# Kernel optimization log

Hardware: AMD Instinct MI355X
Metric: run time of the kernel (lower is better)

The kernel has to match this reference:

```python
import jax, jax.numpy as jnp
import numpy as np

N_MESS = 50000
MAX_NEI = 8
INPUT_SIZE = 128
H_SIZE = 128
DEPTH = 5


def setup_inputs() -> dict:
    key = jax.random.key(0)
    ks = jax.random.split(key, 7)
    s = 0.05
    fmess = jax.random.normal(ks[0], (N_MESS, INPUT_SIZE), dtype=jnp.float32)
    bgraph = jax.random.randint(ks[1], (N_MESS, MAX_NEI), 0, N_MESS, dtype=jnp.int32)
    # torch nn.Linear weights are [out_features, in_features]
    W_z = jax.random.normal(ks[2], (H_SIZE, INPUT_SIZE + H_SIZE), dtype=jnp.float32) * s
    b_z = jnp.zeros((H_SIZE,), jnp.float32)
    W_r = jax.random.normal(ks[3], (H_SIZE, INPUT_SIZE), dtype=jnp.float32) * s  # no bias
    U_r = jax.random.normal(ks[4], (H_SIZE, H_SIZE), dtype=jnp.float32) * s
    b_Ur = jnp.zeros((H_SIZE,), jnp.float32)
    W_h = jax.random.normal(ks[5], (H_SIZE, INPUT_SIZE + H_SIZE), dtype=jnp.float32) * s
    b_h = jnp.zeros((H_SIZE,), jnp.float32)
    return {"fmess": fmess, "bgraph": bgraph, "W_z": W_z, "b_z": b_z,
            "W_r": W_r, "U_r": U_r, "b_Ur": b_Ur, "W_h": W_h, "b_h": b_h}


def _gru_step(fmess, h_nei, W_z, b_z, W_r, U_r, b_Ur, W_h, b_h):
    # h_nei: [N, K, H]
    sum_h = h_nei.sum(axis=1)                                     # [N, H]
    z = jax.nn.sigmoid(jnp.concatenate([fmess, sum_h], axis=1) @ W_z.T + b_z)
    r_1 = (fmess @ W_r.T)[:, None, :]                             # [N, 1, H]
    r_2 = jnp.einsum('nkh,gh->nkg', h_nei, U_r) + b_Ur            # [N, K, H]
    r = jax.nn.sigmoid(r_1 + r_2)
    sum_gated_h = (r * h_nei).sum(axis=1)                         # [N, H]
    pre_h = jnp.tanh(jnp.concatenate([fmess, sum_gated_h], axis=1) @ W_h.T + b_h)
    return (1.0 - z) * sum_h + z * pre_h


def reference(fmess, bgraph, W_z, b_z, W_r, U_r, b_Ur, W_h, b_h):
    n = fmess.shape[0]
    h = jnp.zeros((n, H_SIZE), dtype=fmess.dtype)
    mask = jnp.ones((n, 1), dtype=fmess.dtype).at[0, 0].set(0.0)  # message 0 is padding
    for _ in range(DEPTH):
        h_nei = h[bgraph]                                         # gather: [N, K, H]
        h = _gru_step(fmess, h_nei, W_z, b_z, W_r, U_r, b_Ur, W_h, b_h)
        h = h * mask
    return h
```

## Files before the change

### kernel.cpp

```cpp
#include <hip/hip_runtime.h>
#include <hip/hip_bf16.h>

#define NM 50000
#define HD 128
#define KNEI 8
#define BM 64
#define SPAD 136
#define NBLK ((NM + BM - 1) / BM)
#define NH ((size_t)NM * (size_t)HD)

typedef float  fx4   __attribute__((ext_vector_type(4)));
typedef short  s16x8 __attribute__((ext_vector_type(8)));
typedef short  s16x4 __attribute__((ext_vector_type(4)));

__device__ __forceinline__ float sigm_f(float x) {
    return __builtin_amdgcn_rcpf(1.0f + __expf(-x));
}
__device__ __forceinline__ float tanh_f(float x) {
    return 2.0f * sigm_f(2.0f * x) - 1.0f;
}
__device__ __forceinline__ unsigned short f2b(float f) {
    __hip_bfloat16 h = __float2bfloat16(f);
    return __builtin_bit_cast(unsigned short, h);
}
__device__ __forceinline__ float b2f(unsigned short u) {
    __hip_bfloat16 h = __builtin_bit_cast(__hip_bfloat16, u);
    return __bfloat162float(h);
}

#define MFMA16(a, b, c) __builtin_amdgcn_mfma_f32_16x16x32_bf16(a, b, c, 0, 0, 0)


__device__ __forceinline__ void stage_W16(const unsigned short* __restrict__ W16,
                                          int ldw, int woff,
                                          unsigned short (*Ws)[SPAD], int tid)
{
    const int g  = tid >> 1;
    const int c0 = (tid & 1) << 6;
    const unsigned short* src = W16 + (size_t)g * ldw + woff + c0;
    #pragma unroll
    for (int j = 0; j < 64; j += 8)
        *(s16x8*)&Ws[g][c0 + j] = *(const s16x8*)(src + j);
}

__device__ __forceinline__ void stage_A32(const float* __restrict__ A, int row0,
                                          unsigned short (*As)[SPAD], int tid)
{
    const int r  = tid & 63;
    const int c0 = (tid >> 6) << 5;
    int gr = row0 + r; if (gr >= NM) gr = NM - 1;
    const float* ap = A + (size_t)gr * HD + c0;
    #pragma unroll
    for (int j = 0; j < 32; j += 8) {
        s16x8 s;
        #pragma unroll
        for (int q = 0; q < 8; ++q) s[q] = (short)f2b(ap[j + q]);
        *(s16x8*)&As[r][c0 + j] = s;
    }
}

__device__ __forceinline__ void stage_A16(const unsigned short* __restrict__ A16, int row0,
                                          unsigned short (*As)[SPAD], int tid)
{
    const int r  = tid & 63;
    const int c0 = (tid >> 6) << 5;
    int gr = row0 + r; if (gr >= NM) gr = NM - 1;
    const unsigned short* ap = A16 + (size_t)gr * HD + c0;
    #pragma unroll
    for (int j = 0; j < 32; j += 8)
        *(s16x8*)&As[r][c0 + j] = *(const s16x8*)(ap + j);
}

__device__ __forceinline__ void lds_to_g16(const unsigned short (*L)[SPAD], int row0,
                                           unsigned short* __restrict__ G, int tid)
{
    const int r  = tid & 63;
    const int c0 = (tid >> 6) << 5;
    const int gr = row0 + r;
    if (gr >= NM) return;
    #pragma unroll
    for (int j = 0; j < 32; j += 8)
        *(s16x8*)&G[(size_t)gr * HD + c0 + j] = *(const s16x8*)&L[r][c0 + j];
}

__device__ __forceinline__ void mfma_128(const unsigned short (*As)[SPAD],
                                         const unsigned short (*Ws)[SPAD],
                                         int w, int l, fx4 (&acc)[8])
{
    const int rb = w * 16 + (l & 15);
    const int kq = (l >> 4) << 3;
    #pragma unroll
    for (int ks = 0; ks < 4; ++ks) {
        const s16x8 a = *(const s16x8*)&As[rb][ks * 32 + kq];
        #pragma unroll
        for (int nf = 0; nf < 8; ++nf) {
            const s16x8 b = *(const s16x8*)&Ws[nf * 16 + (l & 15)][ks * 32 + kq];
            acc[nf] = MFMA16(a, b, acc[nf]);
        }
    }
}

#define ZACC(acc) { _Pragma("unroll") for (int z_ = 0; z_ < 8; ++z_) \
                    acc[z_] = (fx4)0.0f; }

__global__ __launch_bounds__(256)
void dgru_wcvt(const float* __restrict__ Wz, const float* __restrict__ Wr,
               const float* __restrict__ Ur, const float* __restrict__ Wh,
               unsigned short* __restrict__ w16)
{
    const int i = blockIdx.x * 256 + threadIdx.x;
    float v;
    if      (i < 32768) v = Wz[i];
    else if (i < 49152) v = Wr[i - 32768];
    else if (i < 65536) v = Ur[i - 49152];
    else                v = Wh[i - 65536];
    w16[i] = f2b(v);
}

__global__ __launch_bounds__(256)
void dgru_pre(const float* __restrict__ fmess,
              const unsigned short* __restrict__ wz16,
              const unsigned short* __restrict__ wr16,
              const unsigned short* __restrict__ wh16,
              const unsigned short* __restrict__ ur16,
              const float* __restrict__ bz, const float* __restrict__ bh,
              const float* __restrict__ bur,
              unsigned short* __restrict__ fmess16,
              unsigned short* __restrict__ pre_r16,
              unsigned short* __restrict__ h16, unsigned short* __restrict__ uh16)
{
    __shared__ unsigned short As[BM][SPAD];
    __shared__ unsigned short Ws[HD][SPAD];
    const int tid  = threadIdx.x;
    const int row0 = blockIdx.x * BM;
    const int w    = tid >> 6;
    const int l    = tid & 63;

    stage_A32(fmess, row0, As, tid);
    stage_W16(wz16, 2 * HD, 0, Ws, tid);
    __syncthreads();

    lds_to_g16(As, row0, fmess16, tid);

    fx4 accz[8]; ZACC(accz);
    mfma_128(As, Ws, w, l, accz);
    __syncthreads();

    stage_W16(wr16, HD, 0, Ws, tid);
    __syncthreads();
    {
        fx4 accr[8]; ZACC(accr);
        mfma_128(As, Ws, w, l, accr);
        __syncthreads();
        #pragma unroll
        for (int nf = 0; nf < 8; ++nf) {
            const int col = nf * 16 + (l & 15);
            #pragma unroll
            for (int q = 0; q < 4; ++q) {
                const int rl = w * 16 + ((l >> 4) << 2) + q;
                Ws[rl][col] = f2b(accr[nf][q]);
            }
        }
        __syncthreads();
        lds_to_g16(Ws, row0, pre_r16, tid);
        __syncthreads();
    }

    stage_W16(wh16, 2 * HD, 0, Ws, tid);
    __syncthreads();
    {
        fx4 acch[8]; ZACC(acch);
        mfma_128(As, Ws, w, l, acch);
        __syncthreads();
        #pragma unroll
        for (int nf = 0; nf < 8; ++nf) {
            const int col = nf * 16 + (l & 15);
            const float bvz = bz[col];
            const float bvh = bh[col];
            #pragma unroll
            for (int q = 0; q < 4; ++q) {
                const int rl = w * 16 + ((l >> 4) << 2) + q;
                const int gr = row0 + rl;
                float h0 = sigm_f(accz[nf][q] + bvz) * tanh_f(acch[nf][q] + bvh);
                if (gr == 0) h0 = 0.0f;
                As[rl][col] = f2b(h0);
            }
        }
    }
    stage_W16(ur16, HD, 0, Ws, tid);
    __syncthreads();

    lds_to_g16(As, row0, h16, tid);
    {
        fx4 accu[8]; ZACC(accu);
        mfma_128(As, Ws, w, l, accu);
        __syncthreads();
        #pragma unroll
        for (int nf = 0; nf < 8; ++nf) {
            const int col = nf * 16 + (l & 15);
            const float bv = bur[col];
            #pragma unroll
            for (int q = 0; q < 4; ++q) {
                const int rl = w * 16 + ((l >> 4) << 2) + q;
                Ws[rl][col] = f2b(accu[nf][q] + bv);
            }
        }
        __syncthreads();
        lds_to_g16(Ws, row0, uh16, tid);
    }
}

__global__ __launch_bounds__(256)
void dgru_gather(const unsigned short* __restrict__ h16,
                 const unsigned short* __restrict__ uh16,
                 const int* __restrict__ bgraph,
                 const unsigned short* __restrict__ pre_r16,
                 unsigned short* __restrict__ sh16, unsigned short* __restrict__ sg16)
{
    const int tid = threadIdx.x;
    const int n   = blockIdx.x * 8 + (tid >> 5);
    const int d0  = (tid & 31) << 2;

    const int4* bg = (const int4*)(bgraph + (size_t)n * KNEI);
    const int4 b0 = bg[0], b1 = bg[1];
    const int idx[KNEI] = {b0.x, b0.y, b0.z, b0.w, b1.x, b1.y, b1.z, b1.w};

    s16x4 hr[KNEI], ur[KNEI];
    #pragma unroll
    for (int k = 0; k < KNEI; ++k)
        hr[k] = *(const s16x4*)&h16[(size_t)idx[k] * HD + d0];
    #pragma unroll
    for (int k = 0; k < KNEI; ++k)
        ur[k] = *(const s16x4*)&uh16[(size_t)idx[k] * HD + d0];
    const s16x4 prb = *(const s16x4*)&pre_r16[(size_t)n * HD + d0];
    float pr[4];
    #pragma unroll
    for (int j = 0; j < 4; ++j) pr[j] = b2f((unsigned short)prb[j]);

    float sh[4] = {0.f, 0.f, 0.f, 0.f};
    float sg[4] = {0.f, 0.f, 0.f, 0.f};
    #pragma unroll
    for (int k = 0; k < KNEI; ++k) {
        #pragma unroll
        for (int j = 0; j < 4; ++j) {
            const float hv = b2f((unsigned short)hr[k][j]);
            const float uv = b2f((unsigned short)ur[k][j]);
            sh[j] += hv;
            sg[j] = fmaf(sigm_f(pr[j] + uv), hv, sg[j]);
        }
    }
    s16x4 osh, osg;
    #pragma unroll
    for (int j = 0; j < 4; ++j) {
        osh[j] = (short)f2b(sh[j]);
        osg[j] = (short)f2b(sg[j]);
    }
    const size_t o = (size_t)n * HD + d0;
    *(s16x4*)&sh16[o] = osh;
    *(s16x4*)&sg16[o] = osg;
}

__global__ __launch_bounds__(256)
void dgru_zh(const unsigned short* __restrict__ fmess16,
             const unsigned short* __restrict__ sh16,
             const unsigned short* __restrict__ sg16,
             const unsigned short* __restrict__ wz16,
             const unsigned short* __restrict__ wh16,
             const unsigned short* __restrict__ ur16,
             const float* __restrict__ bz, const float* __restrict__ bh,
             const float* __restrict__ bur,
             unsigned short* __restrict__ h16, unsigned short* __restrict__ uh16,
             float* __restrict__ hout, int last)
{
    __shared__ unsigned short AsF[BM][SPAD];
    __shared__ unsigned short AsX[BM][SPAD];
    __shared__ unsigned short Ws[HD][SPAD];
    const int tid  = threadIdx.x;
    const int row0 = blockIdx.x * BM;
    const int w    = tid >> 6;
    const int l    = tid & 63;

    stage_A16(fmess16, row0, AsF, tid);
    stage_A16(sh16, row0, AsX, tid);
    stage_W16(wz16, 2 * HD, 0, Ws, tid);
    __syncthreads();
    fx4 acc[8]; ZACC(acc);
    mfma_128(AsF, Ws, w, l, acc);
    __syncthreads();
    stage_W16(wz16, 2 * HD, HD, Ws, tid);
    __syncthreads();
    mfma_128(AsX, Ws, w, l, acc);

    fx4 zres[8];
    float shv[8][4];
    #pragma unroll
    for (int nf = 0; nf < 8; ++nf) {
        const int col = nf * 16 + (l & 15);
        const float bv = bz[col];
        #pragma unroll
        for (int q = 0; q < 4; ++q) {
            const int rl = w * 16 + ((l >> 4) << 2) + q;
            zres[nf][q] = sigm_f(acc[nf][q] + bv);
            shv[nf][q]  = b2f(AsX[rl][col]);
        }
    }
    __syncthreads();

    stage_A16(sg16, row0, AsX, tid);
    stage_W16(wh16, 2 * HD, 0, Ws, tid);
    __syncthreads();
    ZACC(acc);
    mfma_128(AsF, Ws, w, l, acc);
    __syncthreads();
    stage_W16(wh16, 2 * HD, HD, Ws, tid);
    __syncthreads();
    mfma_128(AsX, Ws, w, l, acc);

    #pragma unroll
    for (int nf = 0; nf < 8; ++nf) {
        const int col = nf * 16 + (l & 15);
        const float bv = bh[col];
        #pragma unroll
        for (int q = 0; q < 4; ++q) {
            const int rl = w * 16 + ((l >> 4) << 2) + q;
            const int gr = row0 + rl;
            const float zz = zres[nf][q];
            float o = (1.0f - zz) * shv[nf][q] + zz * tanh_f(acc[nf][q] + bv);
            if (gr == 0) o = 0.0f;
            if (last) {
                if (gr < NM) hout[(size_t)gr * HD + col] = o;
            } else {
                AsF[rl][col] = f2b(o);
            }
        }
    }
    if (last) return;
    __syncthreads();

    stage_W16(ur16, HD, 0, Ws, tid);
    lds_to_g16(AsF, row0, h16, tid);
    __syncthreads();
    ZACC(acc);
    mfma_128(AsF, Ws, w, l, acc);
    #pragma unroll
    for (int nf = 0; nf < 8; ++nf) {
        const int col = nf * 16 + (l & 15);
        const float bv = bur[col];
        #pragma unroll
        for (int q = 0; q < 4; ++q) {
            const int rl = w * 16 + ((l >> 4) << 2) + q;
            AsX[rl][col] = f2b(acc[nf][q] + bv);
        }
    }
    __syncthreads();
    lds_to_g16(AsX, row0, uh16, tid);
}

extern "C" void kernel_launch(void* const* d_in, const int* in_sizes, int n_in,
                              void* d_out, int out_size, void* d_ws, size_t ws_size,
                              hipStream_t stream) {
    const float* fmess  = (const float*)d_in[0];
    const int*   bgraph = (const int*)  d_in[1];
    const float* W_z    = (const float*)d_in[2];
    const float* b_z    = (const float*)d_in[3];
    const float* W_r    = (const float*)d_in[4];
    const float* U_r    = (const float*)d_in[5];
    const float* b_Ur   = (const float*)d_in[6];
    const float* W_h    = (const float*)d_in[7];
    const float* b_h    = (const float*)d_in[8];

    unsigned short* ws16 = (unsigned short*)d_ws;
    unsigned short* fmess16 = ws16;
    unsigned short* pre_r16 = ws16 + NH;
    unsigned short* h16     = ws16 + 2 * NH;
    unsigned short* uh16    = ws16 + 3 * NH;
    unsigned short* sh16    = ws16 + 4 * NH;
    unsigned short* sg16    = ws16 + 5 * NH;
    unsigned short* w16     = ws16 + 6 * NH;
    unsigned short* wz16 = w16;
    unsigned short* wr16 = w16 + 32768;
    unsigned short* ur16 = w16 + 49152;
    unsigned short* wh16 = w16 + 65536;
    float* hout = (float*)d_out;

    dgru_wcvt<<<dim3(384), dim3(256), 0, stream>>>(W_z, W_r, U_r, W_h, w16);

    dgru_pre<<<dim3(NBLK), dim3(256), 0, stream>>>(
        fmess, wz16, wr16, wh16, ur16, b_z, b_h, b_Ur,
        fmess16, pre_r16, h16, uh16);

    for (int it = 1; it < 5; ++it) {
        dgru_gather<<<dim3(NM / 8), dim3(256), 0, stream>>>(
            h16, uh16, bgraph, pre_r16, sh16, sg16);
        dgru_zh<<<dim3(NBLK), dim3(256), 0, stream>>>(
            fmess16, sh16, sg16, wz16, wh16, ur16, b_z, b_h, b_Ur,
            h16, uh16, hout, (it == 4) ? 1 : 0);
    }
}
```

Measured before the change: 338.2 us.

## Hold weight fragments in registers and split GEMM columns across waves

```diff
diff --git a/kernel.cpp b/kernel.cpp
--- a/kernel.cpp
+++ b/kernel.cpp
@@ -30,18 +30,37 @@
 
 #define MFMA16(a, b, c) __builtin_amdgcn_mfma_f32_16x16x32_bf16(a, b, c, 0, 0, 0)
 
-
-__device__ __forceinline__ void stage_W16(const unsigned short* __restrict__ W16,
-                                          int ldw, int woff,
-                                          unsigned short (*Ws)[SPAD], int tid)
-{
-    const int g  = tid >> 1;
-    const int c0 = (tid & 1) << 6;
-    const unsigned short* src = W16 + (size_t)g * ldw + woff + c0;
-    #pragma unroll
-    for (int j = 0; j < 64; j += 8)
-        *(s16x8*)&Ws[g][c0 + j] = *(const s16x8*)(src + j);
-}
+__device__ __forceinline__ void load_bfrag(const unsigned short* __restrict__ W,
+                                           int ldw, int woff, int nf0, int l,
+                                           s16x8 (&bf)[2][4])
+{
+    #pragma unroll
+    for (int j = 0; j < 2; ++j) {
+        const unsigned short* p =
+            W + (size_t)((nf0 + j) * 16 + (l & 15)) * ldw + woff + ((l >> 4) << 3);
+        #pragma unroll
+        for (int ks = 0; ks < 4; ++ks)
+            bf[j][ks] = *(const s16x8*)(p + ks * 32);
+    }
+}
+
+__device__ __forceinline__ void pass(const unsigned short (*As)[SPAD],
+                                     const s16x8 (&bf)[2][4],
+                                     int l, fx4 (&acc)[4][2])
+{
+    const int kq = (l >> 4) << 3;
+    #pragma unroll
+    for (int ks = 0; ks < 4; ++ks)
+        #pragma unroll
+        for (int rb = 0; rb < 4; ++rb) {
+            const s16x8 a = *(const s16x8*)&As[rb * 16 + (l & 15)][ks * 32 + kq];
+            acc[rb][0] = MFMA16(a, bf[0][ks], acc[rb][0]);
+            acc[rb][1] = MFMA16(a, bf[1][ks], acc[rb][1]);
+        }
+}
+
+#define ZACC2(acc) { _Pragma("unroll") for (int z_ = 0; z_ < 4; ++z_) { \
+                     acc[z_][0] = (fx4)0.0f; acc[z_][1] = (fx4)0.0f; } }
 
 __device__ __forceinline__ void stage_A32(const float* __restrict__ A, int row0,
                                           unsigned short (*As)[SPAD], int tid)
@@ -82,26 +101,6 @@
     for (int j = 0; j < 32; j += 8)
         *(s16x8*)&G[(size_t)gr * HD + c0 + j] = *(const s16x8*)&L[r][c0 + j];
 }
-
-__device__ __forceinline__ void mfma_128(const unsigned short (*As)[SPAD],
-                                         const unsigned short (*Ws)[SPAD],
-                                         int w, int l, fx4 (&acc)[8])
-{
-    const int rb = w * 16 + (l & 15);
-    const int kq = (l >> 4) << 3;
-    #pragma unroll
-    for (int ks = 0; ks < 4; ++ks) {
-        const s16x8 a = *(const s16x8*)&As[rb][ks * 32 + kq];
-        #pragma unroll
-        for (int nf = 0; nf < 8; ++nf) {
-            const s16x8 b = *(const s16x8*)&Ws[nf * 16 + (l & 15)][ks * 32 + kq];
-            acc[nf] = MFMA16(a, b, acc[nf]);
-        }
-    }
-}
-
-#define ZACC(acc) { _Pragma("unroll") for (int z_ = 0; z_ < 8; ++z_) \
-                    acc[z_] = (fx4)0.0f; }
 
 __global__ __launch_bounds__(256)
 void dgru_wcvt(const float* __restrict__ Wz, const float* __restrict__ Wr,
@@ -117,7 +116,7 @@
     w16[i] = f2b(v);
 }
 
-__global__ __launch_bounds__(256)
+__global__ __launch_bounds__(256, 3)
 void dgru_pre(const float* __restrict__ fmess,
               const unsigned short* __restrict__ wz16,
               const unsigned short* __restrict__ wr16,
@@ -129,85 +128,82 @@
               unsigned short* __restrict__ pre_r16,
               unsigned short* __restrict__ h16, unsigned short* __restrict__ uh16)
 {
-    __shared__ unsigned short As[BM][SPAD];
-    __shared__ unsigned short Ws[HD][SPAD];
+    __shared__ unsigned short AsF[BM][SPAD];
+    __shared__ unsigned short AsX[BM][SPAD];
     const int tid  = threadIdx.x;
     const int row0 = blockIdx.x * BM;
-    const int w    = tid >> 6;
     const int l    = tid & 63;
-
-    stage_A32(fmess, row0, As, tid);
-    stage_W16(wz16, 2 * HD, 0, Ws, tid);
-    __syncthreads();
-
-    lds_to_g16(As, row0, fmess16, tid);
-
-    fx4 accz[8]; ZACC(accz);
-    mfma_128(As, Ws, w, l, accz);
-    __syncthreads();
-
-    stage_W16(wr16, HD, 0, Ws, tid);
-    __syncthreads();
+    const int nf0  = (tid >> 6) << 1;
+    const int col0 = nf0 * 16 + (l & 15);
+    const int rq   = (l >> 4) << 2;
+
+    s16x8 bfA[2][4], bfB[2][4];
+    load_bfrag(wz16, 2 * HD, 0, nf0, l, bfA);
+    load_bfrag(wr16, HD, 0, nf0, l, bfB);
+    stage_A32(fmess, row0, AsF, tid);
+    __syncthreads();
+
+    lds_to_g16(AsF, row0, fmess16, tid);
+
+    fx4 zacc[4][2]; ZACC2(zacc);
+    pass(AsF, bfA, l, zacc);
+    load_bfrag(wh16, 2 * HD, 0, nf0, l, bfA);
     {
-        fx4 accr[8]; ZACC(accr);
-        mfma_128(As, Ws, w, l, accr);
-        __syncthreads();
-        #pragma unroll
-        for (int nf = 0; nf < 8; ++nf) {
-            const int col = nf * 16 + (l & 15);
+        fx4 racc[4][2]; ZACC2(racc);
+        pass(AsF, bfB, l, racc);
+        #pragma unroll
+        for (int rb = 0; rb < 4; ++rb)
+            #pragma unroll
+            for (int j = 0; j < 2; ++j)
+                #pragma unroll
+                for (int q = 0; q < 4; ++q)
+                    AsX[rb * 16 + rq + q][col0 + j * 16] = f2b(racc[rb][j][q]);
+    }
+    __syncthreads();
+    lds_to_g16(AsX, row0, pre_r16, tid);
+
+    fx4 hacc[4][2]; ZACC2(hacc);
+    pass(AsF, bfA, l, hacc);
+    load_bfrag(ur16, HD, 0, nf0, l, bfB);
+    #pragma unroll
+    for (int rb = 0; rb < 4; ++rb)
+        #pragma unroll
+        for (int j = 0; j < 2; ++j) {
+            const float bvz = bz[col0 + j * 16];
+            const float bvh = bh[col0 + j * 16];
             #pragma unroll
             for (int q = 0; q < 4; ++q) {
-                const int rl = w * 16 + ((l >> 4) << 2) + q;
-                Ws[rl][col] = f2b(accr[nf][q]);
+                const int gr = row0 + rb * 16 + rq + q;
+                float h0 = sigm_f(zacc[rb][j][q] + bvz) * tanh_f(hacc[rb][j][q] + bvh);
+                if (gr == 0) h0 = 0.0f;
+                hacc[rb][j][q] = h0;
             }
         }
-        __syncthreads();
-        lds_to_g16(Ws, row0, pre_r16, tid);
-        __syncthreads();
-    }
-
-    stage_W16(wh16, 2 * HD, 0, Ws, tid);
-    __syncthreads();
+    __syncthreads();
+    #pragma unroll
+    for (int rb = 0; rb < 4; ++rb)
+        #pragma unroll
+        for (int j = 0; j < 2; ++j)
+            #pragma unroll
+            for (int q = 0; q < 4; ++q)
+                AsX[rb * 16 + rq + q][col0 + j * 16] = f2b(hacc[rb][j][q]);
+    __syncthreads();
+    lds_to_g16(AsX, row0, h16, tid);
     {
-        fx4 acch[8]; ZACC(acch);
-        mfma_128(As, Ws, w, l, acch);
-        __syncthreads();
-        #pragma unroll
-        for (int nf = 0; nf < 8; ++nf) {
-            const int col = nf * 16 + (l & 15);
-            const float bvz = bz[col];
-            const float bvh = bh[col];
-            #pragma unroll
-            for (int q = 0; q < 4; ++q) {
-                const int rl = w * 16 + ((l >> 4) << 2) + q;
-                const int gr = row0 + rl;
-                float h0 = sigm_f(accz[nf][q] + bvz) * tanh_f(acch[nf][q] + bvh);
-                if (gr == 0) h0 = 0.0f;
-                As[rl][col] = f2b(h0);
+        fx4 uacc[4][2]; ZACC2(uacc);
+        pass(AsX, bfB, l, uacc);
+        #pragma unroll
+        for (int rb = 0; rb < 4; ++rb)
+            #pragma unroll
+            for (int j = 0; j < 2; ++j) {
+                const float bv = bur[col0 + j * 16];
+                #pragma unroll
+                for (int q = 0; q < 4; ++q)
+                    AsF[rb * 16 + rq + q][col0 + j * 16] = f2b(uacc[rb][j][q] + bv);
             }
-        }
-    }
-    stage_W16(ur16, HD, 0, Ws, tid);
-    __syncthreads();
-
-    lds_to_g16(As, row0, h16, tid);
-    {
-        fx4 accu[8]; ZACC(accu);
-        mfma_128(As, Ws, w, l, accu);
-        __syncthreads();
-        #pragma unroll
-        for (int nf = 0; nf < 8; ++nf) {
-            const int col = nf * 16 + (l & 15);
-            const float bv = bur[col];
-            #pragma unroll
-            for (int q = 0; q < 4; ++q) {
-                const int rl = w * 16 + ((l >> 4) << 2) + q;
-                Ws[rl][col] = f2b(accu[nf][q] + bv);
-            }
-        }
-        __syncthreads();
-        lds_to_g16(Ws, row0, uh16, tid);
-    }
+    }
+    __syncthreads();
+    lds_to_g16(AsF, row0, uh16, tid);
 }
 
 __global__ __launch_bounds__(256)
@@ -260,7 +256,7 @@
     *(s16x4*)&sg16[o] = osg;
 }
 
-__global__ __launch_bounds__(256)
+__global__ __launch_bounds__(256, 3)
 void dgru_zh(const unsigned short* __restrict__ fmess16,
              const unsigned short* __restrict__ sh16,
              const unsigned short* __restrict__ sg16,
@@ -274,83 +270,94 @@
 {
     __shared__ unsigned short AsF[BM][SPAD];
     __shared__ unsigned short AsX[BM][SPAD];
-    __shared__ unsigned short Ws[HD][SPAD];
     const int tid  = threadIdx.x;
     const int row0 = blockIdx.x * BM;
-    const int w    = tid >> 6;
     const int l    = tid & 63;
-
+    const int nf0  = (tid >> 6) << 1;
+    const int col0 = nf0 * 16 + (l & 15);
+    const int rq   = (l >> 4) << 2;
+
+    s16x8 bfA[2][4], bfB[2][4];
+    load_bfrag(wz16, 2 * HD, 0,  nf0, l, bfA);
+    load_bfrag(wz16, 2 * HD, HD, nf0, l, bfB);
     stage_A16(fmess16, row0, AsF, tid);
-    stage_A16(sh16, row0, AsX, tid);
-    stage_W16(wz16, 2 * HD, 0, Ws, tid);
-    __syncthreads();
-    fx4 acc[8]; ZACC(acc);
-    mfma_128(AsF, Ws, w, l, acc);
-    __syncthreads();
-    stage_W16(wz16, 2 * HD, HD, Ws, tid);
-    __syncthreads();
-    mfma_128(AsX, Ws, w, l, acc);
-
-    fx4 zres[8];
-    float shv[8][4];
-    #pragma unroll
-    for (int nf = 0; nf < 8; ++nf) {
-        const int col = nf * 16 + (l & 15);
-        const float bv = bz[col];
-        #pragma unroll
-        for (int q = 0; q < 4; ++q) {
-            const int rl = w * 16 + ((l >> 4) << 2) + q;
-            zres[nf][q] = sigm_f(acc[nf][q] + bv);
-            shv[nf][q]  = b2f(AsX[rl][col]);
-        }
-    }
-    __syncthreads();
-
-    stage_A16(sg16, row0, AsX, tid);
-    stage_W16(wh16, 2 * HD, 0, Ws, tid);
-    __syncthreads();
-    ZACC(acc);
-    mfma_128(AsF, Ws, w, l, acc);
-    __syncthreads();
-    stage_W16(wh16, 2 * HD, HD, Ws, tid);
-    __syncthreads();
-    mfma_128(AsX, Ws, w, l, acc);
-
-    #pragma unroll
-    for (int nf = 0; nf < 8; ++nf) {
-        const int col = nf * 16 + (l & 15);
-        const float bv = bh[col];
-        #pragma unroll
-        for (int q = 0; q < 4; ++q) {
-            const int rl = w * 16 + ((l >> 4) << 2) + q;
-            const int gr = row0 + rl;
-            const float zz = zres[nf][q];
-            float o = (1.0f - zz) * shv[nf][q] + zz * tanh_f(acc[nf][q] + bv);
-            if (gr == 0) o = 0.0f;
-            if (last) {
-                if (gr < NM) hout[(size_t)gr * HD + col] = o;
-            } else {
-                AsF[rl][col] = f2b(o);
+    stage_A16(sh16,    row0, AsX, tid);
+    __syncthreads();
+
+    fx4 zacc[4][2]; ZACC2(zacc);
+    pass(AsF, bfA, l, zacc);
+    pass(AsX, bfB, l, zacc);
+    s16x4 shp[4][2];
+    #pragma unroll
+    for (int rb = 0; rb < 4; ++rb)
+        #pragma unroll
+        for (int j = 0; j < 2; ++j) {
+            const float bv = bz[col0 + j * 16];
+            #pragma unroll
+            for (int q = 0; q < 4; ++q) {
+                shp[rb][j][q] = (short)AsX[rb * 16 + rq + q][col0 + j * 16];
+                zacc[rb][j][q] = sigm_f(zacc[rb][j][q] + bv);
             }
         }
-    }
-    if (last) return;
-    __syncthreads();
-
-    stage_W16(ur16, HD, 0, Ws, tid);
+    load_bfrag(wh16, 2 * HD, 0,  nf0, l, bfA);
+    load_bfrag(wh16, 2 * HD, HD, nf0, l, bfB);
+    __syncthreads();
+    stage_A16(sg16, row0, AsX, tid);
+    __syncthreads();
+
+    fx4 hacc[4][2]; ZACC2(hacc);
+    pass(AsF, bfA, l, hacc);
+    pass(AsX, bfB, l, hacc);
+    #pragma unroll
+    for (int rb = 0; rb < 4; ++rb)
+        #pragma unroll
+        for (int j = 0; j < 2; ++j) {
+            const float bv = bh[col0 + j * 16];
+            #pragma unroll
+            for (int q = 0; q < 4; ++q) {
+                const int gr = row0 + rb * 16 + rq + q;
+                const float zz = zacc[rb][j][q];
+                const float sv = b2f((unsigned short)shp[rb][j][q]);
+                float o = (1.0f - zz) * sv + zz * tanh_f(hacc[rb][j][q] + bv);
+                if (gr == 0) o = 0.0f;
+                hacc[rb][j][q] = o;
+            }
+        }
+    if (last) {
+        #pragma unroll
+        for (int rb = 0; rb < 4; ++rb)
+            #pragma unroll
+            for (int j = 0; j < 2; ++j)
+                #pragma unroll
+                for (int q = 0; q < 4; ++q) {
+                    const int gr = row0 + rb * 16 + rq + q;
+                    if (gr < NM) hout[(size_t)gr * HD + col0 + j * 16] = hacc[rb][j][q];
+                }
+        return;
+    }
+    load_bfrag(ur16, HD, 0, nf0, l, bfA);
+    __syncthreads();
+    #pragma unroll
+    for (int rb = 0; rb < 4; ++rb)
+        #pragma unroll
+        for (int j = 0; j < 2; ++j)
+            #pragma unroll
+            for (int q = 0; q < 4; ++q)
+                AsF[rb * 16 + rq + q][col0 + j * 16] = f2b(hacc[rb][j][q]);
+    __syncthreads();
     lds_to_g16(AsF, row0, h16, tid);
-    __syncthreads();
-    ZACC(acc);
-    mfma_128(AsF, Ws, w, l, acc);
-    #pragma unroll
-    for (int nf = 0; nf < 8; ++nf) {
-        const int col = nf * 16 + (l & 15);
-        const float bv = bur[col];
-        #pragma unroll
-        for (int q = 0; q < 4; ++q) {
-            const int rl = w * 16 + ((l >> 4) << 2) + q;
-            AsX[rl][col] = f2b(acc[nf][q] + bv);
-        }
+    {
+        fx4 uacc[4][2]; ZACC2(uacc);
+        pass(AsF, bfA, l, uacc);
+        #pragma unroll
+        for (int rb = 0; rb < 4; ++rb)
+            #pragma unroll
+            for (int j = 0; j < 2; ++j) {
+                const float bv = bur[col0 + j * 16];
+                #pragma unroll
+                for (int q = 0; q < 4; ++q)
+                    AsX[rb * 16 + rq + q][col0 + j * 16] = f2b(uacc[rb][j][q] + bv);
+            }
     }
     __syncthreads();
     lds_to_g16(AsX, row0, uh16, tid);
```

Result: no change. 336.4 us (-0.5%).
